# Performance work log

Hardware: AMD Instinct MI355X
Metric: run time of the kernel (lower is better)

The kernel has to match this reference:

```python
import jax, jax.numpy as jnp
import numpy as np


def setup_inputs() -> dict:
    key = jax.random.key(0)
    ks = jax.random.split(key, 5)
    B, in_ch, H, W = 8, 256, 128, 128
    C = in_ch // 4
    x = jax.random.normal(ks[0], (B, in_ch, H, W), dtype=jnp.float32)
    # 1x1 conv weights stored as [out_ch, in_ch] (kernel spatial dims are 1)
    w_in = jax.random.normal(ks[1], (C, in_ch), dtype=jnp.float32) * (1.0 / np.sqrt(in_ch))
    b_in = jax.random.normal(ks[2], (C,), dtype=jnp.float32) * 0.01
    w_out = jax.random.normal(ks[3], (in_ch, C), dtype=jnp.float32) * (1.0 / np.sqrt(C))
    b_out = jax.random.normal(ks[4], (in_ch,), dtype=jnp.float32) * 0.01
    detal = jnp.array([0.1], dtype=jnp.float32)
    return {"x": x, "w_in": w_in, "b_in": b_in, "w_out": w_out, "b_out": b_out, "detal": detal}


def _mda(x, w_in, b_in, w_out, b_out, detal):
    # InConv: 1x1 conv == channel GEMM
    inp = jnp.einsum('bihw,oi->bohw', x, w_in) + b_in[None, :, None, None]
    B, C, H, W = inp.shape

    # ---- W branch ----
    # AdaptiveAvgPool2d((None,1)) -> mean over W; softmax over size-1 axis (== ones, kept for faithfulness)
    f_w = jax.nn.softmax(inp.mean(axis=3, keepdims=True), axis=3)          # [B,C,H,1]
    f_w = jnp.transpose(f_w, (0, 3, 1, 2)).reshape(B, C * H, 1)
    Xw = inp.reshape(B, C * H, W)
    Gw = Xw * f_w                                                          # [B,CH,W]
    Tw = jax.nn.softmax(jnp.einsum('bkw,bkv->bwv', Gw, Gw), axis=1)        # [B,W,W], softmax over rows
    Wo = jnp.einsum('bkw,bwv->bkv', Xw, Tw).reshape(B, C, H, W)

    # ---- H branch ----
    f_h = jax.nn.softmax(jnp.transpose(inp, (0, 1, 3, 2)).mean(axis=3, keepdims=True), axis=3)  # [B,C,W,1]
    f_h = jnp.transpose(f_h, (0, 3, 1, 2)).reshape(B, C * W, 1)
    Xh = inp.reshape(B, C * W, H)  # raw .view as in torch (scrambles H/W axes intentionally)
    Gh = Xh * f_h
    Th = jax.nn.softmax(jnp.einsum('bkh,bkg->bhg', Gh, Gh), axis=1)        # [B,H,H]
    Ho = jnp.einsum('bkh,bhg->bkg', Xh, Th).reshape(B, C, H, W)

    # ---- C branch ----
    perm = jnp.transpose(inp, (0, 2, 3, 1))                                # [B,H,W,C]
    f_c = jax.nn.softmax(perm.mean(axis=3, keepdims=True), axis=3)         # [B,H,W,1]
    f_c = jnp.transpose(f_c, (0, 3, 1, 2)).reshape(B, H * W, 1)
    Xc = perm.reshape(B, H * W, C)
    Gc = f_c * Xc
    Tc = jax.nn.softmax(jnp.einsum('bnc,bnd->bcd', Gc, Gc), axis=1)        # [B,C,C]
    # torch does .view(B,C,H,W) on a [B,H*W,C] tensor: raw reshape, NOT a transpose
    Co = jnp.einsum('bnc,bcd->bnd', Xc, Tc).reshape(B, C, H, W)

    s = detal[0] * (Co + Wo + Ho)
    # OuConv 1x1 + residual
    return jnp.einsum('bchw,oc->bohw', s, w_out) + b_out[None, :, None, None] + x


def reference(x, w_in, b_in, w_out, b_out, detal):
    return _mda(x, w_in, b_in, w_out, b_out, detal)
```

## Files before the change

kernel.cpp:

```cpp
#include <hip/hip_runtime.h>
#include <math.h>

#define NB 8
#define IC 256
#define CC 64
#define HH 128
#define WW 128
#define NN (HH*WW)
#define NKW 64
#define NKC 64

typedef _Float16 f16x8 __attribute__((ext_vector_type(8)));
typedef float f32x4 __attribute__((ext_vector_type(4)));

static constexpr size_t SZ_INP  = (size_t)NB * CC * NN;
static constexpr size_t OFF_INP = 0;
static constexpr size_t OFF_S   = OFF_INP + SZ_INP;
static constexpr size_t OFF_PC  = OFF_S + SZ_INP;
static constexpr size_t OFF_TW  = OFF_PC + (size_t)NB * NKC * 4096;
static constexpr size_t OFF_TC  = OFF_TW + (size_t)NB * 16384;
static constexpr size_t OFF_WT  = OFF_TC + (size_t)NB * 4096;
static constexpr size_t OFF_WOT = OFF_WT + 16384;
static constexpr size_t OFF_TWT = OFF_WOT + 16384;
static constexpr size_t OFF_TCT = OFF_TWT + 65536;

__global__ __launch_bounds__(256) void k_wt(
    const float* __restrict__ w_in, const float* __restrict__ w_out,
    _Float16* __restrict__ wh, _Float16* __restrict__ woh)
{
    const int idx = blockIdx.x * 256 + threadIdx.x;
    if (idx < 16384) wh[idx] = (_Float16)w_in[idx];
    else             woh[idx - 16384] = (_Float16)w_out[idx - 16384];
}

__global__ __launch_bounds__(256) void k_inconv(
    const float* __restrict__ x, const _Float16* __restrict__ wh,
    const float* __restrict__ b_in, float* __restrict__ inp)
{
    __shared__ __align__(16) _Float16 wl[64 * 264];
    __shared__ __align__(16) _Float16 xh[32 * 136];
    const int b  = blockIdx.y;
    const int n0 = blockIdx.x * 128;
    const int t  = threadIdx.x;
    const int l  = t & 63, wv = t >> 6;
    const int lr = l & 15, kg = (l >> 4) * 8;

    {
        const int r = t >> 2, c = (t & 3) * 64;
        const uint4* src = (const uint4*)(wh + r * 256 + c);
        uint4* dst = (uint4*)(wl + r * 264 + c);
#pragma unroll
        for (int k = 0; k < 8; k++) dst[k] = src[k];
    }

    f32x4 acc[4][2];
#pragma unroll
    for (int mt = 0; mt < 4; mt++)
#pragma unroll
        for (int nt = 0; nt < 2; nt++) acc[mt][nt] = (f32x4){0.f, 0.f, 0.f, 0.f};

    for (int kc = 0; kc < 8; ++kc) {
        __syncthreads();
        {
            const int i = t >> 3, nq = (t & 7) * 16;
            const float* src = x + ((size_t)b * IC + kc * 32 + i) * NN + n0 + nq;
            const float4 v0 = *(const float4*)(src);
            const float4 v1 = *(const float4*)(src + 4);
            const float4 v2 = *(const float4*)(src + 8);
            const float4 v3 = *(const float4*)(src + 12);
            f16x8 h0, h1;
            h0[0] = (_Float16)v0.x; h0[1] = (_Float16)v0.y;
            h0[2] = (_Float16)v0.z; h0[3] = (_Float16)v0.w;
            h0[4] = (_Float16)v1.x; h0[5] = (_Float16)v1.y;
            h0[6] = (_Float16)v1.z; h0[7] = (_Float16)v1.w;
            h1[0] = (_Float16)v2.x; h1[1] = (_Float16)v2.y;
            h1[2] = (_Float16)v2.z; h1[3] = (_Float16)v2.w;
            h1[4] = (_Float16)v3.x; h1[5] = (_Float16)v3.y;
            h1[6] = (_Float16)v3.z; h1[7] = (_Float16)v3.w;
            *(f16x8*)(xh + i * 136 + nq)     = h0;
            *(f16x8*)(xh + i * 136 + nq + 8) = h1;
        }
        __syncthreads();

        f16x8 bf[2];
#pragma unroll
        for (int nt = 0; nt < 2; ++nt) {
            const int n = wv * 32 + nt * 16 + lr;
#pragma unroll
            for (int j = 0; j < 8; ++j) bf[nt][j] = xh[(kg + j) * 136 + n];
        }
#pragma unroll
        for (int mt = 0; mt < 4; ++mt) {
            const f16x8 af = *(const f16x8*)(wl + (mt * 16 + lr) * 264 + kc * 32 + kg);
            acc[mt][0] = __builtin_amdgcn_mfma_f32_16x16x32_f16(af, bf[0], acc[mt][0], 0, 0, 0);
            acc[mt][1] = __builtin_amdgcn_mfma_f32_16x16x32_f16(af, bf[1], acc[mt][1], 0, 0, 0);
        }
    }

#pragma unroll
    for (int mt = 0; mt < 4; ++mt)
#pragma unroll
        for (int nt = 0; nt < 2; ++nt) {
            const int n = n0 + wv * 32 + nt * 16 + lr;
#pragma unroll
            for (int r = 0; r < 4; ++r) {
                const int o = mt * 16 + (l >> 4) * 4 + r;
                inp[((size_t)b * CC + o) * NN + n] = (float)acc[mt][nt][r] + b_in[o];
            }
        }
}

__global__ __launch_bounds__(256) void k_gramW(const float* __restrict__ inp, float* __restrict__ pW)
{
    __shared__ float xs[32 * 132];
    const int b = blockIdx.y, kc = blockIdx.x;
    const int t = threadIdx.x, tx = t & 15, ty = t >> 4;
    const float* Xb = inp + (size_t)b * CC * NN;
    const int k0 = kc * ((CC * HH) / NKW);

    float acc[8][8];
#pragma unroll
    for (int i = 0; i < 8; i++)
#pragma unroll
        for (int j = 0; j < 8; j++) acc[i][j] = 0.f;

    for (int kk = k0; kk < k0 + (CC * HH) / NKW; kk += 32) {
        __syncthreads();
        {
            const int r = t >> 3, cq = (t & 7) * 16;
            const float* src = Xb + ((size_t)kk + r) * WW + cq;
            float* dst = xs + r * 132 + cq;
#pragma unroll
            for (int j = 0; j < 4; j++)
                *(float4*)(dst + 4 * j) = *(const float4*)(src + 4 * j);
        }
        __syncthreads();
#pragma unroll 8
        for (int k = 0; k < 32; k++) {
            const float* row = xs + k * 132;
            float4 t0 = *(const float4*)(row + ty * 8);
            float4 t1 = *(const float4*)(row + ty * 8 + 4);
            float4 u0 = *(const float4*)(row + tx * 8);
            float4 u1 = *(const float4*)(row + tx * 8 + 4);
            float av[8] = {t0.x, t0.y, t0.z, t0.w, t1.x, t1.y, t1.z, t1.w};
            float bv[8] = {u0.x, u0.y, u0.z, u0.w, u1.x, u1.y, u1.z, u1.w};
#pragma unroll
            for (int i = 0; i < 8; i++)
#pragma unroll
                for (int j = 0; j < 8; j++) acc[i][j] += av[i] * bv[j];
        }
    }
    float* dst = pW + ((size_t)b * NKW + kc) * 16384;
#pragma unroll
    for (int i = 0; i < 8; i++)
#pragma unroll
        for (int j = 0; j < 8; j += 4) {
            float4 v = make_float4(acc[i][j], acc[i][j + 1], acc[i][j + 2], acc[i][j + 3]);
            *(float4*)(dst + (ty * 8 + i) * 128 + tx * 8 + j) = v;
        }
}

__global__ __launch_bounds__(256) void k_redW(const float* __restrict__ pW, float* __restrict__ Tw)
{
    const int b = blockIdx.y;
    const int idx = blockIdx.x * 256 + threadIdx.x;
    const float* p = pW + (size_t)b * NKW * 16384 + idx;
    float acc = 0.f;
#pragma unroll
    for (int k = 0; k < NKW; k++) acc += p[(size_t)k * 16384];
    Tw[(size_t)b * 16384 + idx] = acc;
}

__global__ __launch_bounds__(1024) void k_softW(const float* __restrict__ Tw, _Float16* __restrict__ twt)
{
    __shared__ float red[32 * 33];
    const int b = blockIdx.x, v0 = blockIdx.y * 32;
    const int t = threadIdx.x;
    const int vc = t & 31, wg = t >> 5;
    const float* S = Tw + (size_t)b * 16384 + v0 + vc;

    float v[4];
    float m = -3.4e38f;
#pragma unroll
    for (int j = 0; j < 4; j++) { v[j] = S[(wg * 4 + j) * 128]; m = fmaxf(m, v[j]); }
    red[wg * 33 + vc] = m;
    __syncthreads();
    for (int st = 16; st > 0; st >>= 1) {
        if (wg < st) red[wg * 33 + vc] = fmaxf(red[wg * 33 + vc], red[(wg + st) * 33 + vc]);
        __syncthreads();
    }
    m = red[vc];
    __syncthreads();
    float sum = 0.f;
#pragma unroll
    for (int j = 0; j < 4; j++) { v[j] = __expf(v[j] - m); sum += v[j]; }
    red[wg * 33 + vc] = sum;
    __syncthreads();
    for (int st = 16; st > 0; st >>= 1) {
        if (wg < st) red[wg * 33 + vc] += red[(wg + st) * 33 + vc];
        __syncthreads();
    }
    const float inv = 1.f / red[vc];
    _Float16* dst = twt + (size_t)b * 16384 + (size_t)(v0 + vc) * 128 + wg * 4;
#pragma unroll
    for (int j = 0; j < 4; j++) dst[j] = (_Float16)(v[j] * inv);
}

__global__ __launch_bounds__(256) void k_gramC(const float* __restrict__ inp, float* __restrict__ pC)
{
    __shared__ float xt[32 * 68];
    const int b = blockIdx.y, nc = blockIdx.x;
    const int t = threadIdx.x, tx = t & 15, ty = t >> 4;
    const float* ip = inp + (size_t)b * CC * NN;
    const int n0 = nc * (NN / NKC);

    float acc[4][4];
#pragma unroll
    for (int i = 0; i < 4; i++)
#pragma unroll
        for (int j = 0; j < 4; j++) acc[i][j] = 0.f;

    const int scc = t >> 2;
    const int sn  = (t & 3) * 8;

    for (int nt = 0; nt < NN / NKC; nt += 32) {
        __syncthreads();
        {
            const float* src = ip + (size_t)scc * NN + n0 + nt + sn;
            float v[8];
            *(float4*)(v)     = *(const float4*)(src);
            *(float4*)(v + 4) = *(const float4*)(src + 4);
#pragma unroll
            for (int j = 0; j < 8; j++) xt[(sn + j) * 68 + scc] = v[j];
        }
        __syncthreads();
#pragma unroll 8
        for (int nn = 0; nn < 32; nn++) {
            const float4 a4 = *(const float4*)(xt + nn * 68 + ty * 4);
            const float4 e4 = *(const float4*)(xt + nn * 68 + tx * 4);
            const float av[4] = {a4.x, a4.y, a4.z, a4.w};
            const float ev[4] = {e4.x, e4.y, e4.z, e4.w};
#pragma unroll
            for (int i = 0; i < 4; i++)
#pragma unroll
                for (int j = 0; j < 4; j++) acc[i][j] += av[i] * ev[j];
        }
    }
    float* dst = pC + ((size_t)b * NKC + nc) * 4096;
#pragma unroll
    for (int i = 0; i < 4; i++) {
        float4 v = make_float4(acc[i][0], acc[i][1], acc[i][2], acc[i][3]);
        *(float4*)(dst + (ty * 4 + i) * 64 + tx * 4) = v;
    }
}

__global__ __launch_bounds__(256) void k_redC(const float* __restrict__ pC, float* __restrict__ Tc)
{
    const int b = blockIdx.y;
    const int idx = blockIdx.x * 256 + threadIdx.x;
    const float* p = pC + (size_t)b * NKC * 4096 + idx;
    float acc = 0.f;
#pragma unroll
    for (int k = 0; k < NKC; k++) acc += p[(size_t)k * 4096];
    Tc[(size_t)b * 4096 + idx] = acc;
}

__global__ __launch_bounds__(1024) void k_softC(const float* __restrict__ Tc, _Float16* __restrict__ tct)
{
    __shared__ float red[16 * 65];
    const int b = blockIdx.x;
    const int t = threadIdx.x;
    const int dc = t & 63, cg = t >> 6;
    const float* S = Tc + (size_t)b * 4096 + dc;

    float v[4];
    float m = -3.4e38f;
#pragma unroll
    for (int j = 0; j < 4; j++) { v[j] = S[(cg * 4 + j) * 64]; m = fmaxf(m, v[j]); }
    red[cg * 65 + dc] = m;
    __syncthreads();
    for (int st = 8; st > 0; st >>= 1) {
        if (cg < st) red[cg * 65 + dc] = fmaxf(red[cg * 65 + dc], red[(cg + st) * 65 + dc]);
        __syncthreads();
    }
    m = red[dc];
    __syncthreads();
    float sum = 0.f;
#pragma unroll
    for (int j = 0; j < 4; j++) { v[j] = __expf(v[j] - m); sum += v[j]; }
    red[cg * 65 + dc] = sum;
    __syncthreads();
    for (int st = 8; st > 0; st >>= 1) {
        if (cg < st) red[cg * 65 + dc] += red[(cg + st) * 65 + dc];
        __syncthreads();
    }
    const float inv = 1.f / red[dc];
    _Float16* dst = tct + (size_t)b * 4096 + (size_t)dc * 64 + cg * 4;
#pragma unroll
    for (int j = 0; j < 4; j++) dst[j] = (_Float16)(v[j] * inv);
}

__global__ __launch_bounds__(256) void k_co(
    const float* __restrict__ inp, const _Float16* __restrict__ tct,
    const float* __restrict__ detal, float* __restrict__ s)
{
    __shared__ __align__(16) _Float16 xh[128 * 72];
    __shared__ __align__(16) _Float16 tl[64 * 72];
    const int b  = blockIdx.y;
    const int n0 = blockIdx.x * 128;
    const int t  = threadIdx.x;
    const int l  = t & 63, wv = t >> 6;
    const int lr = l & 15, kg = (l >> 4) * 8;

    {
        const int nn = t & 127, ch = t >> 7;
        const float* src = inp + ((size_t)b * CC + ch * 32) * NN + n0 + nn;
#pragma unroll
        for (int k2 = 0; k2 < 4; ++k2) {
            float f[8];
#pragma unroll
            for (int j = 0; j < 8; ++j) f[j] = src[(size_t)(k2 * 8 + j) * NN];
            f16x8 h;
#pragma unroll
            for (int j = 0; j < 8; ++j) h[j] = (_Float16)f[j];
            *(f16x8*)(xh + nn * 72 + ch * 32 + k2 * 8) = h;
        }
    }
    {
        const int d = t >> 2, cq = (t & 3) * 16;
        const _Float16* src = tct + (size_t)b * 4096 + d * 64 + cq;
        *(uint4*)(tl + d * 72 + cq)     = *(const uint4*)(src);
        *(uint4*)(tl + d * 72 + cq + 8) = *(const uint4*)(src + 8);
    }
    __syncthreads();

    f32x4 acc[2][4];
#pragma unroll
    for (int mt = 0; mt < 2; mt++)
#pragma unroll
        for (int nt = 0; nt < 4; nt++) acc[mt][nt] = (f32x4){0.f, 0.f, 0.f, 0.f};

#pragma unroll
    for (int kc = 0; kc < 2; ++kc) {
        f16x8 bf[4];
#pragma unroll
        for (int nt = 0; nt < 4; ++nt)
            bf[nt] = *(const f16x8*)(tl + (nt * 16 + lr) * 72 + kc * 32 + kg);
#pragma unroll
        for (int mt = 0; mt < 2; ++mt) {
            const f16x8 af = *(const f16x8*)(xh + (wv * 32 + mt * 16 + lr) * 72 + kc * 32 + kg);
#pragma unroll
            for (int nt = 0; nt < 4; ++nt)
                acc[mt][nt] = __builtin_amdgcn_mfma_f32_16x16x32_f16(af, bf[nt], acc[mt][nt], 0, 0, 0);
        }
    }

    const float scl = detal[0];
    float* sb = s + (size_t)b * CC * NN;
#pragma unroll
    for (int mt = 0; mt < 2; ++mt)
#pragma unroll
        for (int nt = 0; nt < 4; ++nt) {
            const int d = nt * 16 + lr;
#pragma unroll
            for (int r = 0; r < 4; ++r) {
                const int n = n0 + wv * 32 + mt * 16 + (l >> 4) * 4 + r;
                sb[(size_t)n * 64 + d] = scl * acc[mt][nt][r];
            }
        }
}

__global__ __launch_bounds__(256) void k_wo(
    const float* __restrict__ inp, const _Float16* __restrict__ twt,
    const float* __restrict__ detal, float* __restrict__ s)
{
    __shared__ __align__(16) _Float16 xh[64 * 136];
    __shared__ __align__(16) _Float16 tl[128 * 136];
    const int b = blockIdx.z, hc = blockIdx.y, c = blockIdx.x;
    const int t = threadIdx.x;
    const int l = t & 63, wv = t >> 6;
    const int lr = l & 15, kg = (l >> 4) * 8;
    const int h0 = hc * 64;

    const float* ip = inp + ((size_t)b * CC + c) * NN + (size_t)h0 * WW;

    {
        const int h = t >> 2, wq = (t & 3) * 32;
        const float* src = ip + (size_t)h * WW + wq;
#pragma unroll
        for (int k2 = 0; k2 < 4; ++k2) {
            const float4 v0 = *(const float4*)(src + k2 * 8);
            const float4 v1 = *(const float4*)(src + k2 * 8 + 4);
            f16x8 h8;
            h8[0] = (_Float16)v0.x; h8[1] = (_Float16)v0.y;
            h8[2] = (_Float16)v0.z; h8[3] = (_Float16)v0.w;
            h8[4] = (_Float16)v1.x; h8[5] = (_Float16)v1.y;
            h8[6] = (_Float16)v1.z; h8[7] = (_Float16)v1.w;
            *(f16x8*)(xh + h * 136 + wq + k2 * 8) = h8;
        }
    }
    {
        const int v = t >> 1, wh2 = (t & 1) * 64;
        const _Float16* src = twt + (size_t)b * 16384 + (size_t)v * 128 + wh2;
        uint4* dst = (uint4*)(tl + v * 136 + wh2);
#pragma unroll
        for (int k = 0; k < 8; ++k) dst[k] = *(const uint4*)(src + 8 * k);
    }
    __syncthreads();

    f32x4 acc[8];
#pragma unroll
    for (int nt = 0; nt < 8; nt++) acc[nt] = (f32x4){0.f, 0.f, 0.f, 0.f};

#pragma unroll
    for (int kc = 0; kc < 4; ++kc) {
        const f16x8 af = *(const f16x8*)(xh + (wv * 16 + lr) * 136 + kc * 32 + kg);
#pragma unroll
        for (int nt = 0; nt < 8; ++nt) {
            const f16x8 bf = *(const f16x8*)(tl + (nt * 16 + lr) * 136 + kc * 32 + kg);
            acc[nt] = __builtin_amdgcn_mfma_f32_16x16x32_f16(af, bf, acc[nt], 0, 0, 0);
        }
    }

    const float sc2 = 2.0f * detal[0];
    float* sp = s + ((size_t)b * CC + c) * NN + (size_t)h0 * WW;
#pragma unroll
    for (int nt = 0; nt < 8; ++nt) {
        const int v = nt * 16 + lr;
#pragma unroll
        for (int r = 0; r < 4; ++r) {
            const int h = wv * 16 + (l >> 4) * 4 + r;
            float* p = sp + (size_t)h * WW + v;
            *p = *p + sc2 * acc[nt][r];
        }
    }
}

__global__ __launch_bounds__(256) void k_outconv(
    const float* __restrict__ s, const _Float16* __restrict__ woh,
    const float* __restrict__ b_out, const float* __restrict__ x,
    float* __restrict__ outp)
{
    __shared__ __align__(16) _Float16 wo[256 * 72];
    __shared__ __align__(16) _Float16 sh[32 * 72];
    const int b  = blockIdx.y;
    const int n0 = blockIdx.x * 64;
    const int t  = threadIdx.x;
    const int l  = t & 63, wv = t >> 6;
    const int lr = l & 15, kg = (l >> 4) * 8;

    {
        const uint4* src = (const uint4*)(woh + t * 64);
        uint4* dst = (uint4*)(wo + t * 72);
#pragma unroll
        for (int k = 0; k < 8; k++) dst[k] = src[k];
    }

    f32x4 acc[4][4];
#pragma unroll
    for (int mt = 0; mt < 4; mt++)
#pragma unroll
        for (int nt = 0; nt < 4; nt++) acc[mt][nt] = (f32x4){0.f, 0.f, 0.f, 0.f};

    for (int kc = 0; kc < 2; ++kc) {
        __syncthreads();
        {
            const int c = t >> 3, n8 = (t & 7) * 8;
            const float* src = s + ((size_t)b * CC + kc * 32 + c) * NN + n0 + n8;
            const float4 v0 = *(const float4*)(src);
            const float4 v1 = *(const float4*)(src + 4);
            f16x8 h;
            h[0] = (_Float16)v0.x; h[1] = (_Float16)v0.y;
            h[2] = (_Float16)v0.z; h[3] = (_Float16)v0.w;
            h[4] = (_Float16)v1.x; h[5] = (_Float16)v1.y;
            h[6] = (_Float16)v1.z; h[7] = (_Float16)v1.w;
            *(f16x8*)(sh + c * 72 + n8) = h;
        }
        __syncthreads();

        f16x8 bf[4];
#pragma unroll
        for (int nt = 0; nt < 4; ++nt) {
            const int n = nt * 16 + lr;
#pragma unroll
            for (int j = 0; j < 8; ++j) bf[nt][j] = sh[(kg + j) * 72 + n];
        }
#pragma unroll
        for (int mt = 0; mt < 4; ++mt) {
            const f16x8 af = *(const f16x8*)(wo + (wv * 64 + mt * 16 + lr) * 72 + kc * 32 + kg);
#pragma unroll
            for (int nt = 0; nt < 4; ++nt)
                acc[mt][nt] = __builtin_amdgcn_mfma_f32_16x16x32_f16(af, bf[nt], acc[mt][nt], 0, 0, 0);
        }
    }

#pragma unroll
    for (int mt = 0; mt < 4; ++mt)
#pragma unroll
        for (int nt = 0; nt < 4; ++nt) {
            const int n = n0 + nt * 16 + lr;
#pragma unroll
            for (int r = 0; r < 4; ++r) {
                const int o = wv * 64 + mt * 16 + (l >> 4) * 4 + r;
                const size_t off = ((size_t)b * IC + o) * NN + n;
                outp[off] = (float)acc[mt][nt][r] + b_out[o] + x[off];
            }
        }
}

extern "C" void kernel_launch(void* const* d_in, const int* in_sizes, int n_in,
                              void* d_out, int out_size, void* d_ws, size_t ws_size,
                              hipStream_t stream)
{
    const float* x     = (const float*)d_in[0];
    const float* w_in  = (const float*)d_in[1];
    const float* b_in  = (const float*)d_in[2];
    const float* w_out = (const float*)d_in[3];
    const float* b_out = (const float*)d_in[4];
    const float* detal = (const float*)d_in[5];
    float* out = (float*)d_out;

    float* ws   = (float*)d_ws;
    float* inp  = ws + OFF_INP;
    float* s    = ws + OFF_S;
    float* pW   = ws + OFF_S;
    float* pC   = ws + OFF_PC;
    float* Tw   = ws + OFF_TW;
    float* Tc   = ws + OFF_TC;
    _Float16* wh  = (_Float16*)(ws + OFF_WT);
    _Float16* woh = (_Float16*)(ws + OFF_WOT);
    _Float16* twt = (_Float16*)(ws + OFF_TWT);
    _Float16* tct = (_Float16*)(ws + OFF_TCT);

    k_wt     <<<dim3(128),              256, 0, stream>>>(w_in, w_out, wh, woh);
    k_inconv <<<dim3(NN / 128, NB),     256, 0, stream>>>(x, wh, b_in, inp);
    k_gramW  <<<dim3(NKW, NB),          256, 0, stream>>>(inp, pW);
    k_redW   <<<dim3(64, NB),           256, 0, stream>>>(pW, Tw);
    k_softW  <<<dim3(NB, 4),           1024, 0, stream>>>(Tw, twt);
    k_gramC  <<<dim3(NKC, NB),          256, 0, stream>>>(inp, pC);
    k_redC   <<<dim3(16, NB),           256, 0, stream>>>(pC, Tc);
    k_softC  <<<dim3(NB),              1024, 0, stream>>>(Tc, tct);
    k_co     <<<dim3(NN / 128, NB),     256, 0, stream>>>(inp, tct, detal, s);
    k_wo     <<<dim3(CC, 2, NB),        256, 0, stream>>>(inp, twt, detal, s);
    k_outconv<<<dim3(NN / 64, NB),      256, 0, stream>>>(s, woh, b_out, x, out);
}
```

Baseline: 413.7 us.

## Store activation tiles N-major in LDS for vector MFMA B-fragment loads

In both the input and output 1x1-conv GEMM kernels, the staged activation tile is now written to shared memory transposed (pixel-major, channel-contiguous), so each MFMA B fragment is one 16-byte LDS read instead of eight strided scalar reads. The input conv processes 64 channels per stage, halving the number of barrier rounds. The output conv loads its whole 64-channel tile once before the loop, removing the per-iteration syncs. In exchange, global loads become scalar per-thread reads strided by channel (still coalesced across lanes), and LDS use for the activation tile grows.

```diff
diff --git a/kernel.cpp b/kernel.cpp
--- a/kernel.cpp
+++ b/kernel.cpp
@@ -38,7 +38,7 @@
     const float* __restrict__ b_in, float* __restrict__ inp)
 {
     __shared__ __align__(16) _Float16 wl[64 * 264];
-    __shared__ __align__(16) _Float16 xh[32 * 136];
+    __shared__ __align__(16) _Float16 xh[128 * 72];
     const int b  = blockIdx.y;
     const int n0 = blockIdx.x * 128;
     const int t  = threadIdx.x;
@@ -59,41 +59,36 @@
 #pragma unroll
         for (int nt = 0; nt < 2; nt++) acc[mt][nt] = (f32x4){0.f, 0.f, 0.f, 0.f};
 
-    for (int kc = 0; kc < 8; ++kc) {
+    for (int kc = 0; kc < 4; ++kc) {
         __syncthreads();
         {
-            const int i = t >> 3, nq = (t & 7) * 16;
-            const float* src = x + ((size_t)b * IC + kc * 32 + i) * NN + n0 + nq;
-            const float4 v0 = *(const float4*)(src);
-            const float4 v1 = *(const float4*)(src + 4);
-            const float4 v2 = *(const float4*)(src + 8);
-            const float4 v3 = *(const float4*)(src + 12);
-            f16x8 h0, h1;
-            h0[0] = (_Float16)v0.x; h0[1] = (_Float16)v0.y;
-            h0[2] = (_Float16)v0.z; h0[3] = (_Float16)v0.w;
-            h0[4] = (_Float16)v1.x; h0[5] = (_Float16)v1.y;
-            h0[6] = (_Float16)v1.z; h0[7] = (_Float16)v1.w;
-            h1[0] = (_Float16)v2.x; h1[1] = (_Float16)v2.y;
-            h1[2] = (_Float16)v2.z; h1[3] = (_Float16)v2.w;
-            h1[4] = (_Float16)v3.x; h1[5] = (_Float16)v3.y;
-            h1[6] = (_Float16)v3.z; h1[7] = (_Float16)v3.w;
-            *(f16x8*)(xh + i * 136 + nq)     = h0;
-            *(f16x8*)(xh + i * 136 + nq + 8) = h1;
-        }
-        __syncthreads();
-
-        f16x8 bf[2];
-#pragma unroll
-        for (int nt = 0; nt < 2; ++nt) {
-            const int n = wv * 32 + nt * 16 + lr;
-#pragma unroll
-            for (int j = 0; j < 8; ++j) bf[nt][j] = xh[(kg + j) * 136 + n];
-        }
-#pragma unroll
-        for (int mt = 0; mt < 4; ++mt) {
-            const f16x8 af = *(const f16x8*)(wl + (mt * 16 + lr) * 264 + kc * 32 + kg);
-            acc[mt][0] = __builtin_amdgcn_mfma_f32_16x16x32_f16(af, bf[0], acc[mt][0], 0, 0, 0);
-            acc[mt][1] = __builtin_amdgcn_mfma_f32_16x16x32_f16(af, bf[1], acc[mt][1], 0, 0, 0);
+            const int nn = t & 127, ch = t >> 7;
+            const float* src = x + ((size_t)b * IC + kc * 64 + ch * 32) * NN + n0 + nn;
+#pragma unroll
+            for (int k2 = 0; k2 < 4; ++k2) {
+                float f[8];
+#pragma unroll
+                for (int j = 0; j < 8; ++j) f[j] = src[(size_t)(k2 * 8 + j) * NN];
+                f16x8 h;
+#pragma unroll
+                for (int j = 0; j < 8; ++j) h[j] = (_Float16)f[j];
+                *(f16x8*)(xh + nn * 72 + ch * 32 + k2 * 8) = h;
+            }
+        }
+        __syncthreads();
+
+#pragma unroll
+        for (int kk = 0; kk < 2; ++kk) {
+            f16x8 bf[2];
+#pragma unroll
+            for (int nt = 0; nt < 2; ++nt)
+                bf[nt] = *(const f16x8*)(xh + (wv * 32 + nt * 16 + lr) * 72 + kk * 32 + kg);
+#pragma unroll
+            for (int mt = 0; mt < 4; ++mt) {
+                const f16x8 af = *(const f16x8*)(wl + (mt * 16 + lr) * 264 + kc * 64 + kk * 32 + kg);
+                acc[mt][0] = __builtin_amdgcn_mfma_f32_16x16x32_f16(af, bf[0], acc[mt][0], 0, 0, 0);
+                acc[mt][1] = __builtin_amdgcn_mfma_f32_16x16x32_f16(af, bf[1], acc[mt][1], 0, 0, 0);
+            }
         }
     }
 
@@ -442,7 +437,7 @@
     float* __restrict__ outp)
 {
     __shared__ __align__(16) _Float16 wo[256 * 72];
-    __shared__ __align__(16) _Float16 sh[32 * 72];
+    __shared__ __align__(16) _Float16 sh[64 * 72];
     const int b  = blockIdx.y;
     const int n0 = blockIdx.x * 64;
     const int t  = threadIdx.x;
@@ -455,6 +450,21 @@
 #pragma unroll
         for (int k = 0; k < 8; k++) dst[k] = src[k];
     }
+    {
+        const int nn = t & 63, ch = t >> 6;
+        const float* src = s + ((size_t)b * CC + ch * 16) * NN + n0 + nn;
+#pragma unroll
+        for (int k2 = 0; k2 < 2; ++k2) {
+            float f[8];
+#pragma unroll
+            for (int j = 0; j < 8; ++j) f[j] = src[(size_t)(k2 * 8 + j) * NN];
+            f16x8 h;
+#pragma unroll
+            for (int j = 0; j < 8; ++j) h[j] = (_Float16)f[j];
+            *(f16x8*)(sh + nn * 72 + ch * 16 + k2 * 8) = h;
+        }
+    }
+    __syncthreads();
 
     f32x4 acc[4][4];
 #pragma unroll
@@ -462,29 +472,12 @@
 #pragma unroll
         for (int nt = 0; nt < 4; nt++) acc[mt][nt] = (f32x4){0.f, 0.f, 0.f, 0.f};
 
+#pragma unroll
     for (int kc = 0; kc < 2; ++kc) {
-        __syncthreads();
-        {
-            const int c = t >> 3, n8 = (t & 7) * 8;
-            const float* src = s + ((size_t)b * CC + kc * 32 + c) * NN + n0 + n8;
-            const float4 v0 = *(const float4*)(src);
-            const float4 v1 = *(const float4*)(src + 4);
-            f16x8 h;
-            h[0] = (_Float16)v0.x; h[1] = (_Float16)v0.y;
-            h[2] = (_Float16)v0.z; h[3] = (_Float16)v0.w;
-            h[4] = (_Float16)v1.x; h[5] = (_Float16)v1.y;
-            h[6] = (_Float16)v1.z; h[7] = (_Float16)v1.w;
-            *(f16x8*)(sh + c * 72 + n8) = h;
-        }
-        __syncthreads();
-
         f16x8 bf[4];
 #pragma unroll
-        for (int nt = 0; nt < 4; ++nt) {
-            const int n = nt * 16 + lr;
-#pragma unroll
-            for (int j = 0; j < 8; ++j) bf[nt][j] = sh[(kg + j) * 72 + n];
-        }
+        for (int nt = 0; nt < 4; ++nt)
+            bf[nt] = *(const f16x8*)(sh + (nt * 16 + lr) * 72 + kc * 32 + kg);
 #pragma unroll
         for (int mt = 0; mt < 4; ++mt) {
             const f16x8 af = *(const f16x8*)(wo + (wv * 64 + mt * 16 + lr) * 72 + kc * 32 + kg);
```

New measurement: 411.7 us. No clear change (-0.5%).
